# Optimization experiments

Hardware: AMD Instinct MI355X
Metric: run time of the kernel (lower is better)

Reference implementation:

```python
import jax, jax.numpy as jnp
import numpy as np

H, B, I = 1024, 64, 128
W_SCALE = 0.192
BETA = 10.0 / W_SCALE   # softplus-like sharpness 'b' in source
DT = 0.1
DELTA_T = 1.0
Z_MIN, Z_MAX = 0.001, 0.1


def setup_inputs() -> dict:
    key = jax.random.key(0)
    ks = jax.random.split(key, 12)
    s = 1.0 / np.sqrt(H)  # nn.init.uniform_(param, -1/sqrt(H), 1/sqrt(H))
    u = lambda k, shp: jax.random.uniform(k, shp, jnp.float32, -s, s)
    return {
        "x": jax.random.normal(ks[0], (I, B), jnp.float32),
        "v_t": jnp.zeros((B, H), jnp.float32),
        "X": jnp.ones((B, H, H), jnp.float32),            # depression state x=1
        "U": jnp.full((B, H, H), 0.9, jnp.float32),       # facilitation state U=0.9
        "raw_w_r": u(ks[1], (H, H)),
        "p_r": u(ks[2], (H, I)),
        "b_r": u(ks[3], (H, 1)),
        "g_z": u(ks[4], (H, 1)),
        "c_x": u(ks[5], (H, H)),
        "c_u": u(ks[6], (H, H)),
        "c_U": u(ks[7], (H, H)),
        "a_exc": jax.random.uniform(ks[8], (), jnp.float32, -s, s),
        "a_inh": jax.random.uniform(ks[9], (), jnp.float32, -s, s),
    }


def reference(x, v_t, X, U, raw_w_r, p_r, b_r, g_z, c_x, c_u, c_U, a_exc, a_inh):
    sig = jax.nn.sigmoid
    # rectified recurrent weights: (1/b) * log(cosh(b * raw)) -- same formula in
    # all four quadrants of the source, so apply it to the whole matrix.
    w_r = jnp.log(jnp.cosh(BETA * raw_w_r)) / BETA          # (H, H), >= 0
    w_z = jnp.abs(w_r)
    p_z = jnp.abs(p_r)
    # Dale gain: excitatory gain for first half of rows, inhibitory for second.
    a = jnp.concatenate([jnp.full((H // 2, 1), 1.0) * a_exc,
                         jnp.full((H // 2, 1), 1.0) * a_inh], axis=0)
    A = 10.0 * sig(a)                                        # (H, 1)

    vt = v_t.T                                               # (H, B)
    r = sig(vt)                                              # (H, B) firing rates
    rb = r.T[:, :, None]                                     # (B, H, 1) -> r_t[j,b]

    # synaptic depression X: X' = z_x + (1-z_x)X - dt * U * X * r_pre
    z_x = Z_MIN + (Z_MAX - Z_MIN) * sig(c_x)                 # (H, H)
    X_new = z_x + (1.0 - z_x) * X - DELTA_T * U * (X * rb)   # (B, H, H)

    # synaptic facilitation U: U' = Ucap*z_u + (1-z_u)U + dt * Ucap * (1-U) * r_pre
    z_u = Z_MIN + (Z_MAX - Z_MIN) * sig(c_u)
    Ucap = 0.9 * sig(c_U)                                    # (H, H)
    U_new = Ucap * z_u + (1.0 - z_u) * U + DELTA_T * Ucap * ((1.0 - U) * rb)
    U_new = jnp.clip(U_new, jax.lax.stop_gradient(Ucap)[None], 1.0)

    # gate z_t = dt * sigmoid(w_z (A*r) + p_z x + g_z)
    z_t = DT * sig(w_z @ (A * r) + p_z @ x + g_z)            # (H, B)

    # membrane update: per-batch effective weights (X*U*w_r) applied to rates
    rec = jnp.einsum('bjk,kb->jb', X_new * U_new * w_r, r)   # (H, B)
    v_new = (1.0 - z_t) * vt + DT * (rec + p_r @ x + b_r)    # (H, B)
    v_new = v_new.T                                          # (B, H)

    return v_new
```

## Files before the change

### kernel.cpp

```cpp
#include <hip/hip_runtime.h>
#include <cstddef>

#define Hdim 1024
#define Bdim 64
#define Idim 128

#define BETA_F 52.083333333333336f
#define INV_BETA_F 0.0192f
#define LN2_F 0.6931471805599453f

__device__ __forceinline__ float sigf(float x) {
    return 1.0f / (1.0f + __expf(-x));
}

__device__ __forceinline__ float logcoshf_(float t) {
    float a = fabsf(t);
    return a + log1pf(__expf(-2.0f * a)) - LN2_F;
}

__global__ void pre_kernel(const float* __restrict__ x,
                           const float* __restrict__ v_t,
                           const float* __restrict__ p_r,
                           const float* __restrict__ b_r,
                           const float* __restrict__ g_z,
                           float* __restrict__ r_ws,
                           float* __restrict__ membx,
                           float* __restrict__ gatex) {
    const int j = blockIdx.x;
    const int b = threadIdx.x;
    const float* pr = p_r + (size_t)j * Idim;
    float accm = 0.0f, accg = 0.0f;
#pragma unroll 4
    for (int i = 0; i < Idim; ++i) {
        float p  = pr[i];
        float xv = x[i * Bdim + b];
        accm = fmaf(p, xv, accm);
        accg = fmaf(fabsf(p), xv, accg);
    }
    membx[j * Bdim + b] = accm + b_r[j];
    gatex[j * Bdim + b] = accg + g_z[j];

    int id = j * Bdim + b;
    r_ws[id] = sigf(v_t[id]);
}

__global__ __launch_bounds__(256, 6) void main_kernel(
    const float* __restrict__ X,
    const float* __restrict__ U,
    const float* __restrict__ raw_w_r,
    const float* __restrict__ c_x,
    const float* __restrict__ c_u,
    const float* __restrict__ c_U,
    const float* __restrict__ v_t,
    const float* __restrict__ a_exc,
    const float* __restrict__ a_inh,
    const float* __restrict__ r_ws,
    const float* __restrict__ membx,
    const float* __restrict__ gatex,
    float* __restrict__ out) {
    const int wave = threadIdx.x >> 6;
    const int lane = threadIdx.x & 63;
    const int j    = blockIdx.y * 4 + wave;
    const int b0   = blockIdx.x * 2;

    const size_t prow = (size_t)j * Hdim;
    const float* pw  = raw_w_r + prow;
    const float* pzx = c_x + prow;
    const float* pzu = c_u + prow;
    const float* puc = c_U + prow;

    const float* X0 = X + ((size_t)b0 * Hdim + j) * Hdim;
    const float* X1 = X0 + (size_t)Hdim * Hdim;
    const float* U0 = U + ((size_t)b0 * Hdim + j) * Hdim;
    const float* U1 = U0 + (size_t)Hdim * Hdim;
    const float* rr0 = r_ws + b0 * Hdim;
    const float* rr1 = rr0 + Hdim;

    const float rj0 = rr0[j];
    const float rj1 = rr1[j];

    float rec0 = 0.f, rec1 = 0.f;
    float ge0 = 0.f, ge1 = 0.f;
    float gi0 = 0.f, gi1 = 0.f;

#pragma unroll
    for (int chunk = 0; chunk < 4; ++chunk) {
        const int k = (chunk * 64 + lane) * 4;
        float4 rw = *(const float4*)(pw + k);
        float4 cx = *(const float4*)(pzx + k);
        float4 cu = *(const float4*)(pzu + k);
        float4 cN = *(const float4*)(puc + k);
        float4 r0 = *(const float4*)(rr0 + k);
        float4 r1 = *(const float4*)(rr1 + k);
        float4 Xv0 = *(const float4*)(X0 + k);
        float4 Uv0 = *(const float4*)(U0 + k);
        float4 Xv1 = *(const float4*)(X1 + k);
        float4 Uv1 = *(const float4*)(U1 + k);

        float4 wr, zx, zu, uc;
        wr.x = logcoshf_(BETA_F * rw.x) * INV_BETA_F;
        wr.y = logcoshf_(BETA_F * rw.y) * INV_BETA_F;
        wr.z = logcoshf_(BETA_F * rw.z) * INV_BETA_F;
        wr.w = logcoshf_(BETA_F * rw.w) * INV_BETA_F;
        zx.x = 0.001f + 0.099f * sigf(cx.x);
        zx.y = 0.001f + 0.099f * sigf(cx.y);
        zx.z = 0.001f + 0.099f * sigf(cx.z);
        zx.w = 0.001f + 0.099f * sigf(cx.w);
        zu.x = 0.001f + 0.099f * sigf(cu.x);
        zu.y = 0.001f + 0.099f * sigf(cu.y);
        zu.z = 0.001f + 0.099f * sigf(cu.z);
        zu.w = 0.001f + 0.099f * sigf(cu.w);
        uc.x = 0.9f * sigf(cN.x);
        uc.y = 0.9f * sigf(cN.y);
        uc.z = 0.9f * sigf(cN.z);
        uc.w = 0.9f * sigf(cN.w);

        float g0 = 0.f, g1 = 0.f;
#define COMPONENT(c)                                                          \
    {                                                                         \
        float xn0 = zx.c + (1.0f - zx.c) * Xv0.c - Uv0.c * Xv0.c * rj0;       \
        float un0 = uc.c * zu.c + (1.0f - zu.c) * Uv0.c +                     \
                    uc.c * (1.0f - Uv0.c) * rj0;                              \
        un0 = fminf(fmaxf(un0, uc.c), 1.0f);                                  \
        rec0 = fmaf(xn0 * un0 * wr.c, r0.c, rec0);                            \
        g0   = fmaf(wr.c, r0.c, g0);                                          \
        float xn1 = zx.c + (1.0f - zx.c) * Xv1.c - Uv1.c * Xv1.c * rj1;       \
        float un1 = uc.c * zu.c + (1.0f - zu.c) * Uv1.c +                     \
                    uc.c * (1.0f - Uv1.c) * rj1;                              \
        un1 = fminf(fmaxf(un1, uc.c), 1.0f);                                  \
        rec1 = fmaf(xn1 * un1 * wr.c, r1.c, rec1);                            \
        g1   = fmaf(wr.c, r1.c, g1);                                          \
    }
        COMPONENT(x)
        COMPONENT(y)
        COMPONENT(z)
        COMPONENT(w)
#undef COMPONENT
        if (chunk < 2) { ge0 += g0; ge1 += g1; }
        else           { gi0 += g0; gi1 += g1; }
    }

    const float Aexc = 10.0f * sigf(a_exc[0]);
    const float Ainh = 10.0f * sigf(a_inh[0]);
    float gate0 = fmaf(Aexc, ge0, Ainh * gi0);
    float gate1 = fmaf(Aexc, ge1, Ainh * gi1);

#pragma unroll
    for (int off = 32; off > 0; off >>= 1) {
        rec0  += __shfl_xor(rec0, off, 64);
        rec1  += __shfl_xor(rec1, off, 64);
        gate0 += __shfl_xor(gate0, off, 64);
        gate1 += __shfl_xor(gate1, off, 64);
    }

    if (lane == 0) {
        {
            float z  = 0.1f * sigf(gate0 + gatex[j * Bdim + b0]);
            float vt = v_t[(size_t)b0 * Hdim + j];
            out[(size_t)b0 * Hdim + j] =
                (1.0f - z) * vt + 0.1f * (rec0 + membx[j * Bdim + b0]);
        }
        {
            const int b = b0 + 1;
            float z  = 0.1f * sigf(gate1 + gatex[j * Bdim + b]);
            float vt = v_t[(size_t)b * Hdim + j];
            out[(size_t)b * Hdim + j] =
                (1.0f - z) * vt + 0.1f * (rec1 + membx[j * Bdim + b]);
        }
    }
}

extern "C" void kernel_launch(void* const* d_in, const int* in_sizes, int n_in,
                              void* d_out, int out_size, void* d_ws, size_t ws_size,
                              hipStream_t stream) {
    const float* x       = (const float*)d_in[0];
    const float* v_t     = (const float*)d_in[1];
    const float* X       = (const float*)d_in[2];
    const float* U       = (const float*)d_in[3];
    const float* raw_w_r = (const float*)d_in[4];
    const float* p_r     = (const float*)d_in[5];
    const float* b_r     = (const float*)d_in[6];
    const float* g_z     = (const float*)d_in[7];
    const float* c_x     = (const float*)d_in[8];
    const float* c_u     = (const float*)d_in[9];
    const float* c_U     = (const float*)d_in[10];
    const float* a_exc   = (const float*)d_in[11];
    const float* a_inh   = (const float*)d_in[12];

    float* out = (float*)d_out;

    float* r_ws  = (float*)d_ws;
    float* membx = r_ws + Bdim * Hdim;
    float* gatex = membx + Hdim * Bdim;

    pre_kernel<<<dim3(Hdim), dim3(Bdim), 0, stream>>>(
        x, v_t, p_r, b_r, g_z, r_ws, membx, gatex);

    main_kernel<<<dim3(Bdim / 2, Hdim / 4), dim3(256), 0, stream>>>(
        X, U, raw_w_r, c_x, c_u, c_U, v_t, a_exc, a_inh,
        r_ws, membx, gatex, out);
}
```

Measured before the change: 577.2 us.

## Precompute per-row weight transforms in shared memory and reuse across batches

Restructures main_kernel so each block owns one row j and sixteen batches. It computes the log-cosh weight and the three sigmoid gates for that row once into shared memory, and each wave then processes two batch pairs reading those cached values. This removes the repeated per-batch transcendental work, which dominated the previous version. It also switches to faster rcp/log intrinsics and raises the occupancy hint. The trade-offs are slightly lower accuracy from the fast math and fewer waves streaming X/U per row concurrently.

```diff
diff --git a/kernel.cpp b/kernel.cpp
--- a/kernel.cpp
+++ b/kernel.cpp
@@ -13,9 +13,13 @@
     return 1.0f / (1.0f + __expf(-x));
 }
 
-__device__ __forceinline__ float logcoshf_(float t) {
+__device__ __forceinline__ float sigf_fast(float x) {
+    return __builtin_amdgcn_rcpf(1.0f + __expf(-x));
+}
+
+__device__ __forceinline__ float logcoshf_fast(float t) {
     float a = fabsf(t);
-    return a + log1pf(__expf(-2.0f * a)) - LN2_F;
+    return a + __logf(1.0f + __expf(-2.0f * a)) - LN2_F;
 }
 
 __global__ void pre_kernel(const float* __restrict__ x,
@@ -44,7 +48,7 @@
     r_ws[id] = sigf(v_t[id]);
 }
 
-__global__ __launch_bounds__(256, 6) void main_kernel(
+__global__ __launch_bounds__(256, 8) void main_kernel(
     const float* __restrict__ X,
     const float* __restrict__ U,
     const float* __restrict__ raw_w_r,
@@ -58,64 +62,82 @@
     const float* __restrict__ membx,
     const float* __restrict__ gatex,
     float* __restrict__ out) {
-    const int wave = threadIdx.x >> 6;
-    const int lane = threadIdx.x & 63;
-    const int j    = blockIdx.y * 4 + wave;
-    const int b0   = blockIdx.x * 2;
-
-    const size_t prow = (size_t)j * Hdim;
-    const float* pw  = raw_w_r + prow;
-    const float* pzx = c_x + prow;
-    const float* pzu = c_u + prow;
-    const float* puc = c_U + prow;
-
-    const float* X0 = X + ((size_t)b0 * Hdim + j) * Hdim;
-    const float* X1 = X0 + (size_t)Hdim * Hdim;
-    const float* U0 = U + ((size_t)b0 * Hdim + j) * Hdim;
-    const float* U1 = U0 + (size_t)Hdim * Hdim;
-    const float* rr0 = r_ws + b0 * Hdim;
-    const float* rr1 = rr0 + Hdim;
-
-    const float rj0 = rr0[j];
-    const float rj1 = rr1[j];
-
-    float rec0 = 0.f, rec1 = 0.f;
-    float ge0 = 0.f, ge1 = 0.f;
-    float gi0 = 0.f, gi1 = 0.f;
+    __shared__ __align__(16) float s_zx[Hdim];
+    __shared__ __align__(16) float s_zu[Hdim];
+    __shared__ __align__(16) float s_uc[Hdim];
+    __shared__ __align__(16) float s_wr[Hdim];
+
+    const int j   = blockIdx.y;
+    const int tid = threadIdx.x;
+
+    {
+        const int k = tid * 4;
+        const size_t ro = (size_t)j * Hdim + k;
+        float4 rw = *(const float4*)(raw_w_r + ro);
+        float4 cx = *(const float4*)(c_x + ro);
+        float4 cu = *(const float4*)(c_u + ro);
+        float4 cN = *(const float4*)(c_U + ro);
+
+        s_wr[k + 0] = logcoshf_fast(BETA_F * rw.x) * INV_BETA_F;
+        s_wr[k + 1] = logcoshf_fast(BETA_F * rw.y) * INV_BETA_F;
+        s_wr[k + 2] = logcoshf_fast(BETA_F * rw.z) * INV_BETA_F;
+        s_wr[k + 3] = logcoshf_fast(BETA_F * rw.w) * INV_BETA_F;
+
+        s_zx[k + 0] = 0.001f + 0.099f * sigf_fast(cx.x);
+        s_zx[k + 1] = 0.001f + 0.099f * sigf_fast(cx.y);
+        s_zx[k + 2] = 0.001f + 0.099f * sigf_fast(cx.z);
+        s_zx[k + 3] = 0.001f + 0.099f * sigf_fast(cx.w);
+
+        s_zu[k + 0] = 0.001f + 0.099f * sigf_fast(cu.x);
+        s_zu[k + 1] = 0.001f + 0.099f * sigf_fast(cu.y);
+        s_zu[k + 2] = 0.001f + 0.099f * sigf_fast(cu.z);
+        s_zu[k + 3] = 0.001f + 0.099f * sigf_fast(cu.w);
+
+        s_uc[k + 0] = 0.9f * sigf_fast(cN.x);
+        s_uc[k + 1] = 0.9f * sigf_fast(cN.y);
+        s_uc[k + 2] = 0.9f * sigf_fast(cN.z);
+        s_uc[k + 3] = 0.9f * sigf_fast(cN.w);
+    }
+    __syncthreads();
+
+    const int wave  = tid >> 6;
+    const int lane  = tid & 63;
+    const int bbase = blockIdx.x * 16 + wave * 4;
+
+    const float Aexc = 10.0f * sigf(a_exc[0]);
+    const float Ainh = 10.0f * sigf(a_inh[0]);
+
+    for (int pair = 0; pair < 2; ++pair) {
+        const int b0 = bbase + 2 * pair;
+        const float* X0 = X + ((size_t)b0 * Hdim + j) * Hdim;
+        const float* X1 = X0 + (size_t)Hdim * Hdim;
+        const float* U0 = U + ((size_t)b0 * Hdim + j) * Hdim;
+        const float* U1 = U0 + (size_t)Hdim * Hdim;
+        const float* rr0 = r_ws + b0 * Hdim;
+        const float* rr1 = rr0 + Hdim;
+
+        const float rj0 = rr0[j];
+        const float rj1 = rr1[j];
+
+        float rec0 = 0.f, rec1 = 0.f;
+        float ge0 = 0.f, ge1 = 0.f;
+        float gi0 = 0.f, gi1 = 0.f;
 
 #pragma unroll
-    for (int chunk = 0; chunk < 4; ++chunk) {
-        const int k = (chunk * 64 + lane) * 4;
-        float4 rw = *(const float4*)(pw + k);
-        float4 cx = *(const float4*)(pzx + k);
-        float4 cu = *(const float4*)(pzu + k);
-        float4 cN = *(const float4*)(puc + k);
-        float4 r0 = *(const float4*)(rr0 + k);
-        float4 r1 = *(const float4*)(rr1 + k);
-        float4 Xv0 = *(const float4*)(X0 + k);
-        float4 Uv0 = *(const float4*)(U0 + k);
-        float4 Xv1 = *(const float4*)(X1 + k);
-        float4 Uv1 = *(const float4*)(U1 + k);
-
-        float4 wr, zx, zu, uc;
-        wr.x = logcoshf_(BETA_F * rw.x) * INV_BETA_F;
-        wr.y = logcoshf_(BETA_F * rw.y) * INV_BETA_F;
-        wr.z = logcoshf_(BETA_F * rw.z) * INV_BETA_F;
-        wr.w = logcoshf_(BETA_F * rw.w) * INV_BETA_F;
-        zx.x = 0.001f + 0.099f * sigf(cx.x);
-        zx.y = 0.001f + 0.099f * sigf(cx.y);
-        zx.z = 0.001f + 0.099f * sigf(cx.z);
-        zx.w = 0.001f + 0.099f * sigf(cx.w);
-        zu.x = 0.001f + 0.099f * sigf(cu.x);
-        zu.y = 0.001f + 0.099f * sigf(cu.y);
-        zu.z = 0.001f + 0.099f * sigf(cu.z);
-        zu.w = 0.001f + 0.099f * sigf(cu.w);
-        uc.x = 0.9f * sigf(cN.x);
-        uc.y = 0.9f * sigf(cN.y);
-        uc.z = 0.9f * sigf(cN.z);
-        uc.w = 0.9f * sigf(cN.w);
-
-        float g0 = 0.f, g1 = 0.f;
+        for (int chunk = 0; chunk < 4; ++chunk) {
+            const int k = chunk * 256 + lane * 4;
+            float4 Xv0 = *(const float4*)(X0 + k);
+            float4 Uv0 = *(const float4*)(U0 + k);
+            float4 Xv1 = *(const float4*)(X1 + k);
+            float4 Uv1 = *(const float4*)(U1 + k);
+            float4 r0  = *(const float4*)(rr0 + k);
+            float4 r1  = *(const float4*)(rr1 + k);
+            float4 zx  = *(const float4*)(s_zx + k);
+            float4 zu  = *(const float4*)(s_zu + k);
+            float4 uc  = *(const float4*)(s_uc + k);
+            float4 wr  = *(const float4*)(s_wr + k);
+
+            float g0 = 0.f, g1 = 0.f;
 #define COMPONENT(c)                                                          \
     {                                                                         \
         float xn0 = zx.c + (1.0f - zx.c) * Xv0.c - Uv0.c * Xv0.c * rj0;       \
@@ -131,41 +153,40 @@
         rec1 = fmaf(xn1 * un1 * wr.c, r1.c, rec1);                            \
         g1   = fmaf(wr.c, r1.c, g1);                                          \
     }
-        COMPONENT(x)
-        COMPONENT(y)
-        COMPONENT(z)
-        COMPONENT(w)
+            COMPONENT(x)
+            COMPONENT(y)
+            COMPONENT(z)
+            COMPONENT(w)
 #undef COMPONENT
-        if (chunk < 2) { ge0 += g0; ge1 += g1; }
-        else           { gi0 += g0; gi1 += g1; }
-    }
-
-    const float Aexc = 10.0f * sigf(a_exc[0]);
-    const float Ainh = 10.0f * sigf(a_inh[0]);
-    float gate0 = fmaf(Aexc, ge0, Ainh * gi0);
-    float gate1 = fmaf(Aexc, ge1, Ainh * gi1);
+            if (chunk < 2) { ge0 += g0; ge1 += g1; }
+            else           { gi0 += g0; gi1 += g1; }
+        }
+
+        float gate0 = fmaf(Aexc, ge0, Ainh * gi0);
+        float gate1 = fmaf(Aexc, ge1, Ainh * gi1);
 
 #pragma unroll
-    for (int off = 32; off > 0; off >>= 1) {
-        rec0  += __shfl_xor(rec0, off, 64);
-        rec1  += __shfl_xor(rec1, off, 64);
-        gate0 += __shfl_xor(gate0, off, 64);
-        gate1 += __shfl_xor(gate1, off, 64);
-    }
-
-    if (lane == 0) {
-        {
-            float z  = 0.1f * sigf(gate0 + gatex[j * Bdim + b0]);
-            float vt = v_t[(size_t)b0 * Hdim + j];
-            out[(size_t)b0 * Hdim + j] =
-                (1.0f - z) * vt + 0.1f * (rec0 + membx[j * Bdim + b0]);
+        for (int off = 32; off > 0; off >>= 1) {
+            rec0  += __shfl_xor(rec0, off, 64);
+            rec1  += __shfl_xor(rec1, off, 64);
+            gate0 += __shfl_xor(gate0, off, 64);
+            gate1 += __shfl_xor(gate1, off, 64);
         }
-        {
-            const int b = b0 + 1;
-            float z  = 0.1f * sigf(gate1 + gatex[j * Bdim + b]);
-            float vt = v_t[(size_t)b * Hdim + j];
-            out[(size_t)b * Hdim + j] =
-                (1.0f - z) * vt + 0.1f * (rec1 + membx[j * Bdim + b]);
+
+        if (lane == 0) {
+            {
+                float z  = 0.1f * sigf(gate0 + gatex[j * Bdim + b0]);
+                float vt = v_t[(size_t)b0 * Hdim + j];
+                out[(size_t)b0 * Hdim + j] =
+                    (1.0f - z) * vt + 0.1f * (rec0 + membx[j * Bdim + b0]);
+            }
+            {
+                const int b = b0 + 1;
+                float z  = 0.1f * sigf(gate1 + gatex[j * Bdim + b]);
+                float vt = v_t[(size_t)b * Hdim + j];
+                out[(size_t)b * Hdim + j] =
+                    (1.0f - z) * vt + 0.1f * (rec1 + membx[j * Bdim + b]);
+            }
         }
     }
 }
@@ -196,7 +217,7 @@
     pre_kernel<<<dim3(Hdim), dim3(Bdim), 0, stream>>>(
         x, v_t, p_r, b_r, g_z, r_ws, membx, gatex);
 
-    main_kernel<<<dim3(Bdim / 2, Hdim / 4), dim3(256), 0, stream>>>(
+    main_kernel<<<dim3(4, Hdim), dim3(256), 0, stream>>>(
         X, U, raw_w_r, c_x, c_u, c_U, v_t, a_exc, a_inh,
         r_ws, membx, gatex, out);
 }
```

After: 779.5 us. 35.0% more time.
